# Performance work log

Measured on AMD Instinct MI355X. Metric: run time of the kernel, lower is better.

Reference implementation:

```python
import jax, jax.numpy as jnp
import numpy as np

D_MODEL = 512
D_STATE = 16
D_INNER = 2 * D_MODEL  # expand_factor=2
IN_CH = 256
B_SZ, H_SZ, W_SZ = 4, 32, 32


def setup_inputs() -> dict:
    key = jax.random.key(0)
    ks = jax.random.split(key, 24)
    f = jax.random.normal
    inp = {}
    inp["x_V"] = f(ks[0], (B_SZ, IN_CH, H_SZ, W_SZ), jnp.float32)
    inp["x_I"] = f(ks[1], (B_SZ, IN_CH, H_SZ, W_SZ), jnp.float32)
    # channel_reduce: 1x1 conv + BN (inference stats)
    inp["conv_red_w"] = f(ks[2], (D_MODEL, IN_CH), jnp.float32) * 0.05
    inp["bn_red_g"] = jnp.ones((D_MODEL,), jnp.float32)
    inp["bn_red_b"] = jnp.zeros((D_MODEL,), jnp.float32)
    inp["bn_red_m"] = jnp.zeros((D_MODEL,), jnp.float32)
    inp["bn_red_v"] = jnp.ones((D_MODEL,), jnp.float32)
    # channel_restore: 1x1 conv + BN
    inp["conv_res_w"] = f(ks[3], (IN_CH, D_MODEL), jnp.float32) * 0.05
    inp["bn_res_g"] = jnp.ones((IN_CH,), jnp.float32)
    inp["bn_res_b"] = jnp.zeros((IN_CH,), jnp.float32)
    inp["bn_res_m"] = jnp.zeros((IN_CH,), jnp.float32)
    inp["bn_res_v"] = jnp.ones((IN_CH,), jnp.float32)
    # lambda_predictor convs (1x1 on pooled features == linear)
    inp["lam_w1"] = f(ks[4], (D_MODEL // 4, D_MODEL * 2), jnp.float32) * 0.05
    inp["lam_b1"] = jnp.zeros((D_MODEL // 4,), jnp.float32)
    inp["lam_w2"] = f(ks[5], (2, D_MODEL // 4), jnp.float32) * 0.05
    inp["lam_b2"] = jnp.zeros((2,), jnp.float32)
    # two SimplifiedMamba2Blocks
    for i, p in enumerate(["V", "I"]):
        kk = jax.random.split(ks[6 + i], 6)
        inp[p + "_in_w"] = f(kk[0], (2 * D_INNER, D_MODEL), jnp.float32) * 0.03
        inp[p + "_out_w"] = f(kk[1], (D_MODEL, D_INNER), jnp.float32) * 0.03
        # A = -exp(A_log) in (-1, -0.05): stable decay
        inp[p + "_A_log"] = jnp.log(jax.random.uniform(kk[2], (D_INNER, D_STATE), jnp.float32, 0.05, 0.95))
        inp[p + "_B"] = f(kk[3], (D_INNER, D_STATE), jnp.float32) * 0.05
        inp[p + "_C"] = jnp.full((D_INNER, D_STATE), 0.01, jnp.float32)
        inp[p + "_ln_g"] = jnp.ones((D_MODEL,), jnp.float32)
        inp[p + "_ln_b"] = jnp.zeros((D_MODEL,), jnp.float32)
    inp["gate"] = jnp.asarray(0.1, jnp.float32)
    return inp


def _bn(x, g, b, m, v):
    # x: (B,C,H,W); inference-mode batchnorm
    return (x - m[:, None, None]) / jnp.sqrt(v[:, None, None] + 1e-5) * g[:, None, None] + b[:, None, None]


def _conv1x1(x, w):
    return jnp.einsum('bchw,oc->bohw', x, w)


def _ssm_scan(x_ssm, A, Bm, Cm, reverse):
    # x_ssm: (B,L,I); A,Bm,Cm: (I,S)
    bsz = x_ssm.shape[0]
    h0 = jnp.zeros((bsz, A.shape[0], A.shape[1]), x_ssm.dtype)

    def step(h, xt):  # xt: (B,I)
        h = jnp.clip(h * A + xt[:, :, None] * Bm, -10.0, 10.0)
        return h, jnp.einsum('bis,is->bi', h, Cm)

    _, ys = jax.lax.scan(step, h0, jnp.swapaxes(x_ssm, 0, 1), reverse=reverse)
    return jnp.swapaxes(ys, 0, 1)  # (B,L,I), in original time order


def _mamba(x, ln_g, ln_b, in_w, out_w, A_log, Bm, Cm):
    # LayerNorm
    mu = jnp.mean(x, -1, keepdims=True)
    var = jnp.mean((x - mu) ** 2, -1, keepdims=True)
    xn = (x - mu) / jnp.sqrt(var + 1e-5) * ln_g + ln_b
    xp = xn @ in_w.T  # (B,L,2*I)
    x_ssm, gate = jnp.split(xp, 2, axis=-1)
    A = jnp.clip(-jnp.exp(A_log), -10.0, -0.01)
    yf = _ssm_scan(x_ssm, A, Bm, Cm, False)
    yb = _ssm_scan(x_ssm, A, Bm, Cm, True)
    out = 0.5 * (yf + yb) * jax.nn.silu(gate)
    return out @ out_w.T


def reference(x_V, x_I, conv_red_w, bn_red_g, bn_red_b, bn_red_m, bn_red_v,
              conv_res_w, bn_res_g, bn_res_b, bn_res_m, bn_res_v,
              lam_w1, lam_b1, lam_w2, lam_b2,
              V_in_w, V_out_w, V_A_log, V_B, V_C, V_ln_g, V_ln_b,
              I_in_w, I_out_w, I_A_log, I_B, I_C, I_ln_g, I_ln_b, gate):
    B, _, H, W = x_V.shape
    xVr = jax.nn.relu(_bn(_conv1x1(x_V, conv_red_w), bn_red_g, bn_red_b, bn_red_m, bn_red_v))
    xIr = jax.nn.relu(_bn(_conv1x1(x_I, conv_red_w), bn_red_g, bn_red_b, bn_red_m, bn_red_v))
    # same spatial size -> adaptive pooling and [:B] slicing are identities
    conc = jnp.concatenate([xVr, xIr], axis=1)  # (B, 2*d_model, H, W)

    def lam(c):
        p = jnp.mean(c, axis=(2, 3))  # global avg pool -> (B, 2*d_model)
        h1 = jax.nn.relu(p @ lam_w1.T + lam_b1)
        return jax.nn.softmax(h1 @ lam_w2.T + lam_b2, axis=-1)  # (B,2)

    lamV = lam(conc)
    lamI = lam(conc)

    seq_V = jnp.swapaxes(xVr.reshape(B, D_MODEL, H * W), 1, 2)  # (B,L,D)
    seq_I = jnp.swapaxes(xIr.reshape(B, D_MODEL, H * W), 1, 2)

    outV_std = _mamba(seq_V, V_ln_g, V_ln_b, V_in_w, V_out_w, V_A_log, V_B, V_C)
    outI_std = _mamba(seq_I, I_ln_g, I_ln_b, I_in_w, I_out_w, I_A_log, I_B, I_C)
    outV_cross = _mamba(seq_V, V_ln_g, V_ln_b, V_in_w, V_out_w, V_A_log, jax.lax.stop_gradient(I_B), V_C)
    outI_cross = _mamba(seq_I, I_ln_g, I_ln_b, I_in_w, I_out_w, I_A_log, jax.lax.stop_gradient(V_B), I_C)

    outV = lamV[:, 0][:, None, None] * outV_std + lamV[:, 1][:, None, None] * outV_cross
    outI = lamI[:, 0][:, None, None] * outI_std + lamI[:, 1][:, None, None] * outI_cross

    featV = jnp.swapaxes(outV, 1, 2).reshape(B, D_MODEL, H, W)
    featI = jnp.swapaxes(outI, 1, 2).reshape(B, D_MODEL, H, W)
    featV = _bn(_conv1x1(featV, conv_res_w), bn_res_g, bn_res_b, bn_res_m, bn_res_v)
    featI = _bn(_conv1x1(featI, conv_res_w), bn_res_g, bn_res_b, bn_res_m, bn_res_v)

    g = jax.nn.sigmoid(gate)
    return (x_V + g * featV, x_I + g * featI)
```

## Files before the change

### kernel.cpp

```cpp
#include <hip/hip_runtime.h>
#include <hip/hip_bf16.h>
#include <math.h>

#define L_SZ 1024
#define DM   512
#define DI   1024
#define NS   16
#define CH   256

typedef float4 f4;
typedef __attribute__((ext_vector_type(8))) short short8;
typedef __attribute__((ext_vector_type(8))) unsigned short u16x8;
typedef __attribute__((ext_vector_type(4))) float f32x4;

__device__ __forceinline__ float bf2f(ushort u) {
    union { unsigned int i; float f; } x; x.i = ((unsigned int)u) << 16; return x.f;
}
__device__ __forceinline__ ushort f2bf(float f) {
    union { float f; unsigned int i; } x; x.f = f;
    unsigned int r = x.i + 0x7FFFu + ((x.i >> 16) & 1u);
    return (ushort)(r >> 16);
}
__device__ __forceinline__ uint pkbf(float a, float b) {
    union { __hip_bfloat162 h; uint u; } c;
    c.h = __float22bfloat162_rn(make_float2(a, b));
    return c.u;
}

#define GLOAD16(gp, lp) \
  __builtin_amdgcn_global_load_lds((const __attribute__((address_space(1))) void*)(gp), \
                                   (__attribute__((address_space(3))) void*)(lp), 16, 0, 0)

__global__ __launch_bounds__(256) void k_prep(
    const float* __restrict__ s0, const float* __restrict__ s1,
    const float* __restrict__ s2, const float* __restrict__ s3,
    const float* __restrict__ s4, const float* __restrict__ s5,
    ushort* __restrict__ d0, ushort* __restrict__ d1,
    ushort* __restrict__ d2, ushort* __restrict__ d3,
    ushort* __restrict__ d4, ushort* __restrict__ d5,
    const float* __restrict__ xv, const float* __restrict__ xi,
    ushort* __restrict__ xtv, ushort* __restrict__ xti,
    float* __restrict__ p, unsigned int* __restrict__ cnt)
{
    __shared__ float tile[32][36];
    const int bid = blockIdx.x;
    const int t = threadIdx.x;
    if (bid < 2304) {
        const float* s; ushort* d; int rel;
        if      (bid < 128)  { s = s0; d = d0; rel = bid; }
        else if (bid < 256)  { s = s1; d = d1; rel = bid - 128; }
        else if (bid < 1280) { s = s2; d = d2; rel = bid - 256; }
        else                 { s = s3; d = d3; rel = bid - 1280; }
        const int i = rel * 256 + t;
        f4 v = ((const f4*)s)[i];
        ushort4 o;
        o.x = f2bf(v.x); o.y = f2bf(v.y); o.z = f2bf(v.z); o.w = f2bf(v.w);
        ((ushort4*)d)[i] = o;
        return;
    }
    if (bid < 3328) {
        const int rel = (bid < 2816) ? bid - 2304 : bid - 2816;
        const float* wo = (bid < 2816) ? s4 : s5;
        ushort* wt      = (bid < 2816) ? d4 : d5;
        const int kt = rel & 31, dt = rel >> 5;
        const int d0_ = dt * 32, k0 = kt * 32;
        {
            int cc = t >> 3, ll4 = (t & 7) << 2;
            f4 v = *(const f4*)(wo + (size_t)(d0_ + cc) * 1024 + k0 + ll4);
            tile[cc][ll4 + 0] = v.x; tile[cc][ll4 + 1] = v.y;
            tile[cc][ll4 + 2] = v.z; tile[cc][ll4 + 3] = v.w;
        }
        __syncthreads();
        {
            int ll = t >> 3, cc4 = (t & 7) << 2;
            ushort4 o;
            o.x = f2bf(tile[cc4 + 0][ll]); o.y = f2bf(tile[cc4 + 1][ll]);
            o.z = f2bf(tile[cc4 + 2][ll]); o.w = f2bf(tile[cc4 + 3][ll]);
            *(ushort4*)(wt + (size_t)(k0 + ll) * 512 + d0_ + cc4) = o;
        }
        return;
    }
    if (bid < 5376) {
        const int rel = bid - 3328;
        const int l0 = (rel & 31) * 32, c0 = ((rel >> 5) & 7) * 32;
        const int z = rel >> 8;
        const int b = z & 3, st = z >> 2;
        const float* x = st ? xi : xv;
        ushort* xt = st ? xti : xtv;
        {
            int cc = t >> 3, ll4 = (t & 7) << 2;
            f4 v = *(const f4*)(x + ((size_t)(b * CH + c0 + cc)) * L_SZ + l0 + ll4);
            tile[cc][ll4 + 0] = v.x; tile[cc][ll4 + 1] = v.y;
            tile[cc][ll4 + 2] = v.z; tile[cc][ll4 + 3] = v.w;
        }
        __syncthreads();
        {
            int ll = t >> 3, cc4 = (t & 7) << 2;
            ushort4 o;
            o.x = f2bf(tile[cc4 + 0][ll]); o.y = f2bf(tile[cc4 + 1][ll]);
            o.z = f2bf(tile[cc4 + 2][ll]); o.w = f2bf(tile[cc4 + 3][ll]);
            *(ushort4*)(xt + ((size_t)(b * L_SZ + l0 + ll)) * CH + c0 + cc4) = o;
        }
        return;
    }
    const f4 z4 = {0.f, 0.f, 0.f, 0.f};
    ((f4*)p)[t]       = z4;
    ((f4*)p)[t + 256] = z4;
    ((f4*)p)[t + 512] = z4;
    ((f4*)p)[t + 768] = z4;
    if (t == 0) *cnt = 0u;
}

template<int MODE, int BM, int BN, int OS>
__global__ __launch_bounds__(256) void k_gemm(
    const ushort* __restrict__ A0, const ushort* __restrict__ A1,
    const ushort* __restrict__ B0, const ushort* __restrict__ B1,
    int K,
    float* __restrict__ o0, float* __restrict__ o1,
    ushort* __restrict__ ob0, ushort* __restrict__ ob1,
    ushort* __restrict__ sb0, ushort* __restrict__ sb1,
    const float* __restrict__ pg, const float* __restrict__ pb,
    const float* __restrict__ pm, const float* __restrict__ pv,
    const float* __restrict__ x0, const float* __restrict__ x1,
    const float* __restrict__ gate, float* __restrict__ pp)
{
    constexpr int MT   = BM / 32;
    constexpr int NT   = BN / 32;
    constexpr int ASEG = BM / 16;
    constexpr int NSEG = (BM + BN) / 16;
    constexpr int SPW  = NSEG / 4;
    __shared__ __align__(16) ushort Sl[(BM + BN) * 32];
    const int t = threadIdx.x;
    const int wv = t >> 6, lane = t & 63;
    const int n0 = blockIdx.x * BN, m0 = blockIdx.y * BM;
    const int st = blockIdx.z;
    const ushort* Ap = st ? A1 : A0;
    const ushort* Bp = st ? B1 : B0;
    const int wm = wv >> 1, wn = wv & 1;
    const int lrow = lane & 15, q = lane >> 4;
    f32x4 acc[MT][NT];
    #pragma unroll
    for (int a_ = 0; a_ < MT; ++a_)
        #pragma unroll
        for (int b_ = 0; b_ < NT; ++b_)
            acc[a_][b_] = (f32x4){0.f, 0.f, 0.f, 0.f};
    const int srow = lane >> 2;
    const int skk  = (((lane & 3) ^ ((lane >> 3) & 3)) << 3);
    const int koff = ((q ^ ((lrow >> 1) & 3)) << 3);
    for (int k0 = 0; k0 < K; k0 += 32) {
        #pragma unroll
        for (int s2 = 0; s2 < SPW; ++s2) {
            const int seg = wv * SPW + s2;
            const int grow = (seg < ASEG) ? (m0 + seg * 16 + srow)
                                          : (n0 + (seg - ASEG) * 16 + srow);
            const ushort* src = (seg < ASEG) ? Ap : Bp;
            GLOAD16(src + (size_t)grow * K + k0 + skk, &Sl[seg * 512]);
        }
        __syncthreads();
        short8 af[MT], bfr[NT];
        #pragma unroll
        for (int mt = 0; mt < MT; ++mt)
            af[mt] = *(const short8*)&Sl[(wm * (MT * 16) + mt * 16 + lrow) * 32 + koff];
        #pragma unroll
        for (int nt = 0; nt < NT; ++nt)
            bfr[nt] = *(const short8*)&Sl[(BM + wn * (NT * 16) + nt * 16 + lrow) * 32 + koff];
        #pragma unroll
        for (int mt = 0; mt < MT; ++mt)
            #pragma unroll
            for (int nt = 0; nt < NT; ++nt)
                acc[mt][nt] = __builtin_amdgcn_mfma_f32_16x16x32_bf16(af[mt], bfr[nt], acc[mt][nt], 0, 0, 0);
        __syncthreads();
    }
    if (MODE == 0) {
        ushort* sq = st ? ob1 : ob0;
        const int b = m0 >> 10;
        #pragma unroll
        for (int nt = 0; nt < NT; ++nt) {
            const int gn = n0 + wn * (NT * 16) + nt * 16 + lrow;
            const float s  = pg[gn] * rsqrtf(pv[gn] + 1e-5f);
            const float sh = pb[gn] - pm[gn] * s;
            float psum = 0.f;
            #pragma unroll
            for (int mt = 0; mt < MT; ++mt) {
                const int gm = m0 + wm * (MT * 16) + mt * 16 + q * 4;
                float v[4];
                #pragma unroll
                for (int r = 0; r < 4; ++r) {
                    v[r] = fmaxf(fmaf(acc[mt][nt][r], s, sh), 0.f);
                    psum += v[r];
                }
                const uint u01 = pkbf(v[0], v[1]);
                const uint u23 = pkbf(v[2], v[3]);
                ushort* bp = sq + (size_t)gm * DM + gn;
                bp[0]      = (ushort)u01;
                bp[DM]     = (ushort)(u01 >> 16);
                bp[2 * DM] = (ushort)u23;
                bp[3 * DM] = (ushort)(u23 >> 16);
            }
            psum += __shfl_xor(psum, 16, 64);
            psum += __shfl_xor(psum, 32, 64);
            if (q == 0)
                atomicAdd(pp + (b * 1024 + st * 512 + gn), psum * (1.0f / 1024.0f));
        }
    } else if (MODE == 1) {
        const bool isx = (n0 < 1024);
        ushort* xp = st ? ob1 : ob0;
        ushort* sp = st ? sb1 : sb0;
        #pragma unroll
        for (int nt = 0; nt < NT; ++nt) {
            const int gn = n0 + wn * (NT * 16) + nt * 16 + lrow;
            #pragma unroll
            for (int mt = 0; mt < MT; ++mt) {
                const int gm = m0 + wm * (MT * 16) + mt * 16 + q * 4;
                if (isx) {
                    const uint u01 = pkbf(acc[mt][nt][0], acc[mt][nt][1]);
                    const uint u23 = pkbf(acc[mt][nt][2], acc[mt][nt][3]);
                    ushort* bp = xp + (size_t)gm * DI + gn;
                    bp[0]      = (ushort)u01;
                    bp[DI]     = (ushort)(u01 >> 16);
                    bp[2 * DI] = (ushort)u23;
                    bp[3 * DI] = (ushort)(u23 >> 16);
                } else {
                    float sv[4];
                    #pragma unroll
                    for (int r = 0; r < 4; ++r) {
                        const float v = acc[mt][nt][r];
                        sv[r] = v / (1.f + __expf(-v));
                    }
                    const uint u01 = pkbf(sv[0], sv[1]);
                    const uint u23 = pkbf(sv[2], sv[3]);
                    ushort* bp = sp + (size_t)gm * DI + gn - 1024;
                    bp[0]      = (ushort)u01;
                    bp[DI]     = (ushort)(u01 >> 16);
                    bp[2 * DI] = (ushort)u23;
                    bp[3 * DI] = (ushort)(u23 >> 16);
                }
            }
        }
    } else if (MODE == 2) {
        ushort* fp_ = st ? ob1 : ob0;
        #pragma unroll
        for (int nt = 0; nt < NT; ++nt) {
            const int gn = n0 + wn * (NT * 16) + nt * 16 + lrow;
            #pragma unroll
            for (int mt = 0; mt < MT; ++mt) {
                const int gm = m0 + wm * (MT * 16) + mt * 16 + q * 4;
                const uint u01 = pkbf(acc[mt][nt][0], acc[mt][nt][1]);
                const uint u23 = pkbf(acc[mt][nt][2], acc[mt][nt][3]);
                ushort* bp = fp_ + (size_t)gm * OS + gn;
                bp[0]      = (ushort)u01;
                bp[OS]     = (ushort)(u01 >> 16);
                bp[2 * OS] = (ushort)u23;
                bp[3 * OS] = (ushort)(u23 >> 16);
            }
        }
    } else {
        const float* xin = st ? x1 : x0;
        float* op = st ? o1 : o0;
        const float g = 1.f / (1.f + __expf(-gate[0]));
        #pragma unroll
        for (int nt = 0; nt < NT; ++nt) {
            const int gn = n0 + wn * (NT * 16) + nt * 16 + lrow;
            const float s  = pg[gn] * rsqrtf(pv[gn] + 1e-5f);
            const float sh = pb[gn] - pm[gn] * s;
            #pragma unroll
            for (int mt = 0; mt < MT; ++mt) {
                const int gmb = m0 + wm * (MT * 16) + mt * 16 + q * 4;
                const int b = gmb >> 10, l = gmb & 1023;
                const size_t off = ((size_t)(b * CH + gn)) * L_SZ + l;
                f4 xi = *(const f4*)(xin + off);
                f4 o;
                o.x = xi.x + g * fmaf(acc[mt][nt][0], s, sh);
                o.y = xi.y + g * fmaf(acc[mt][nt][1], s, sh);
                o.z = xi.z + g * fmaf(acc[mt][nt][2], s, sh);
                o.w = xi.w + g * fmaf(acc[mt][nt][3], s, sh);
                *(f4*)(op + off) = o;
            }
        }
    }
}

__global__ __launch_bounds__(256) void k_lam(
    const float* __restrict__ p, const float* __restrict__ w1,
    const float* __restrict__ b1, const float* __restrict__ w2,
    const float* __restrict__ b2, float* __restrict__ h1,
    float* __restrict__ lam, unsigned int* __restrict__ cnt)
{
    __shared__ float lsm[8];
    __shared__ unsigned int tick;
    const int t = threadIdx.x, lane = t & 63, wv = t >> 6;
    const int idx = blockIdx.x * 4 + wv;
    const int b = idx >> 7, j = idx & 127;
    const float* pb = p + b * 1024;
    const float* wr = w1 + j * 1024;
    float s = 0.f;
    #pragma unroll
    for (int k = 0; k < 16; ++k)
        s = fmaf(pb[lane + k * 64], wr[lane + k * 64], s);
    #pragma unroll
    for (int off = 1; off < 64; off <<= 1) s += __shfl_xor(s, off, 64);
    if (lane == 0) h1[idx] = fmaxf(s + b1[j], 0.f);
    __threadfence();
    __syncthreads();
    if (t == 0) tick = atomicAdd(cnt, 1u);
    __syncthreads();
    if (tick != 127u) return;
    __threadfence();
    {
        const int g32 = t >> 5, l32 = t & 31;
        const int bb = g32 >> 1, kk = g32 & 1;
        const float* hb = h1 + bb * 128;
        const float* wr2 = w2 + kk * 128;
        float ss = 0.f;
        #pragma unroll
        for (int u = 0; u < 4; ++u)
            ss = fmaf(hb[l32 + u * 32], wr2[l32 + u * 32], ss);
        #pragma unroll
        for (int off = 1; off < 32; off <<= 1) ss += __shfl_xor(ss, off, 64);
        if (l32 == 0) lsm[g32] = ss + b2[kk];
    }
    __syncthreads();
    if (t < 4) {
        const float a0 = lsm[t * 2], a1 = lsm[t * 2 + 1];
        const float m  = fmaxf(a0, a1);
        const float e0 = __expf(a0 - m), e1 = __expf(a1 - m);
        const float inv = 1.f / (e0 + e1);
        lam[t * 2 + 0] = e0 * inv;
        lam[t * 2 + 1] = e1 * inv;
    }
}

__global__ __launch_bounds__(256) void k_ln(
    const ushort* __restrict__ seq0, const ushort* __restrict__ seq1,
    const float* __restrict__ g0, const float* __restrict__ b0,
    const float* __restrict__ g1, const float* __restrict__ b1,
    ushort* __restrict__ ln0, ushort* __restrict__ ln1)
{
    const int t = threadIdx.x, lane = t & 63, wv = t >> 6;
    const int row = blockIdx.x * 4 + wv, st = blockIdx.y;
    const ushort* seq = st ? seq1 : seq0;
    const float* gg  = st ? g1 : g0;
    const float* bb  = st ? b1 : b0;
    ushort* ln = st ? ln1 : ln0;
    const u16x8 v = *(const u16x8*)(seq + (size_t)row * DM + lane * 8);
    float f[8];
    float s = 0.f, ss = 0.f;
    #pragma unroll
    for (int i = 0; i < 8; ++i) {
        f[i] = bf2f(v[i]);
        s += f[i];
        ss = fmaf(f[i], f[i], ss);
    }
    #pragma unroll
    for (int off = 1; off < 64; off <<= 1) {
        s += __shfl_xor(s, off, 64); ss += __shfl_xor(ss, off, 64);
    }
    const float mu = s * (1.f / 512.f);
    const float rstd = rsqrtf(ss * (1.f / 512.f) - mu * mu + 1e-5f);
    const f4 gv0 = *(const f4*)(gg + lane * 8);
    const f4 gv1 = *(const f4*)(gg + lane * 8 + 4);
    const f4 bv0 = *(const f4*)(bb + lane * 8);
    const f4 bv1 = *(const f4*)(bb + lane * 8 + 4);
    const float gvv[8] = {gv0.x, gv0.y, gv0.z, gv0.w, gv1.x, gv1.y, gv1.z, gv1.w};
    const float bvv[8] = {bv0.x, bv0.y, bv0.z, bv0.w, bv1.x, bv1.y, bv1.z, bv1.w};
    u16x8 o;
    #pragma unroll
    for (int i = 0; i < 8; i += 2) {
        const uint u = pkbf(fmaf((f[i]     - mu) * rstd, gvv[i],     bvv[i]),
                            fmaf((f[i + 1] - mu) * rstd, gvv[i + 1], bvv[i + 1]));
        o[i]     = (ushort)u;
        o[i + 1] = (ushort)(u >> 16);
    }
    *(u16x8*)(ln + (size_t)row * DM + lane * 8) = o;
}

__global__ __launch_bounds__(128) void k_scan(
    const ushort* __restrict__ xsV, const ushort* __restrict__ xsI,
    const ushort* __restrict__ sgV, const ushort* __restrict__ sgI,
    const float* __restrict__ VA, const float* __restrict__ VB,
    const float* __restrict__ VC, const float* __restrict__ IA,
    const float* __restrict__ IB, const float* __restrict__ IC,
    const float* __restrict__ lam,
    ushort* __restrict__ yV, ushort* __restrict__ yI)
{
    __shared__ __align__(16) ushort xf[2][16][64];
    __shared__ __align__(16) ushort xb[2][16][64];
    __shared__ ushort yfb[32][64];
    __shared__ ushort ybb[32][64];
    const int t = threadIdx.x;
    const int shalf = t & 1;
    const int il = t >> 1;
    const int b = blockIdx.y;
    const int st = blockIdx.z >> 4, j = blockIdx.z & 15;
    const int c0 = blockIdx.x * 64;
    const ushort* xrow  = (st ? xsI : xsV) + (size_t)b * L_SZ * DI + c0;
    const ushort* sgrow = (st ? sgI : sgV) + (size_t)b * L_SZ * DI + c0;
    ushort* yrow        = (st ? yI  : yV ) + (size_t)b * L_SZ * DI + c0;
    const float* Alog = st ? IA : VA;
    const float* Cm   = st ? IC : VC;
    const float* Bown = st ? IB : VB;
    const float* Both = st ? VB : IB;
    const float lam0 = lam[b * 2 + 0], lam1 = lam[b * 2 + 1];
    float a[8], w[8], gf[8], gb[8];
    const int base = (c0 + il) * NS + shalf * 8;
    #pragma unroll
    for (int s = 0; s < 8; ++s) {
        a[s] = fminf(fmaxf(-__expf(Alog[base + s]), -10.f), -0.01f);
        w[s] = 0.5f * Cm[base + s] * fmaf(lam0, Bown[base + s], lam1 * Both[base + s]);
        gf[s] = 0.f; gb[s] = 0.f;
    }
    const int row0 = j << 6;
    const int srow = t >> 3;
    const int scol = (t & 7) << 3;
    {
        int rf = row0 - 64 + srow;          rf = max(0, min(1023, rf));
        GLOAD16(xrow + (size_t)rf * DI + scol, &xf[0][srow][0]);
        int rb = row0 + 127 - srow;         rb = max(0, min(1023, rb));
        GLOAD16(xrow + (size_t)rb * DI + scol, &xb[0][srow][0]);
    }
    __syncthreads();
    for (int si = 0; si < 8; ++si) {
        const int buf = si & 1;
        if (si < 7) {
            const int base2 = (si + 1) * 16;
            int rf = row0 - 64 + base2 + srow;  rf = max(0, min(1023, rf));
            GLOAD16(xrow + (size_t)rf * DI + scol, &xf[buf ^ 1][srow][0]);
            int rb = row0 + 127 - base2 - srow; rb = max(0, min(1023, rb));
            GLOAD16(xrow + (size_t)rb * DI + scol, &xb[buf ^ 1][srow][0]);
        }
        if (si == 4) {
            if (j == 0) {
                for (int s = 0; s < 8; ++s) gf[s] = 0.f;
            }
            if (j == 15) {
                for (int s = 0; s < 8; ++s) gb[s] = 0.f;
            }
        }
        if (si < 4) {
            #pragma unroll
            for (int n = 0; n < 16; ++n) {
                const float vf = bf2f(xf[buf][n][il]);
                const float vb = bf2f(xb[buf][n][il]);
                #pragma unroll
                for (int s = 0; s < 8; ++s) {
                    gf[s] = fmaf(a[s], gf[s], vf);
                    gb[s] = fmaf(a[s], gb[s], vb);
                }
            }
        } else if (si < 6) {
            const int mb = (si - 4) * 16;
            #pragma unroll
            for (int n = 0; n < 16; ++n) {
                const float vf = bf2f(xf[buf][n][il]);
                const float vb = bf2f(xb[buf][n][il]);
                float yf = 0.f, yb = 0.f;
                #pragma unroll
                for (int s = 0; s < 8; ++s) {
                    gf[s] = fmaf(a[s], gf[s], vf);
                    yf    = fmaf(gf[s], w[s], yf);
                    gb[s] = fmaf(a[s], gb[s], vb);
                    yb    = fmaf(gb[s], w[s], yb);
                }
                yf += __shfl_xor(yf, 1, 64);
                yb += __shfl_xor(yb, 1, 64);
                const int m = mb + n;
                ushort* qq = shalf ? &ybb[31 - m][0] : &yfb[m][0];
                qq[il] = f2bf(shalf ? yb : yf);
            }
        } else {
            const int mb = (si - 6) * 16 + 32;
            #pragma unroll
            for (int n = 0; n < 16; ++n) {
                const float vf = bf2f(xf[buf][n][il]);
                const float vb = bf2f(xb[buf][n][il]);
                float yf = 0.f, yb = 0.f;
                #pragma unroll
                for (int s = 0; s < 8; ++s) {
                    gf[s] = fmaf(a[s], gf[s], vf);
                    yf    = fmaf(gf[s], w[s], yf);
                    gb[s] = fmaf(a[s], gb[s], vb);
                    yb    = fmaf(gb[s], w[s], yb);
                }
                yf += __shfl_xor(yf, 1, 64);
                yb += __shfl_xor(yb, 1, 64);
                const int m = mb + n;
                const int rF = row0 + m;
                const int rB = row0 + 63 - m;
                const int r  = shalf ? rB : rF;
                const ushort* pq = shalf ? &yfb[63 - m][0] : &ybb[m - 32][0];
                const float own  = shalf ? yb : yf;
                const float z = (own + bf2f(pq[il]))
                              * bf2f(sgrow[(size_t)r * DI + il]);
                yrow[(size_t)r * DI + il] = f2bf(z);
            }
        }
        __syncthreads();
    }
}

extern "C" void kernel_launch(void* const* d_in, const int* in_sizes, int n_in,
                              void* d_out, int out_size, void* d_ws, size_t ws_size,
                              hipStream_t stream)
{
    const float* xV       = (const float*)d_in[0];
    const float* xI       = (const float*)d_in[1];
    const float* convredw = (const float*)d_in[2];
    const float* bnredg   = (const float*)d_in[3];
    const float* bnredb   = (const float*)d_in[4];
    const float* bnredm   = (const float*)d_in[5];
    const float* bnredv   = (const float*)d_in[6];
    const float* convresw = (const float*)d_in[7];
    const float* bnresg   = (const float*)d_in[8];
    const float* bnresb   = (const float*)d_in[9];
    const float* bnresm   = (const float*)d_in[10];
    const float* bnresv   = (const float*)d_in[11];
    const float* lamw1    = (const float*)d_in[12];
    const float* lamb1    = (const float*)d_in[13];
    const float* lamw2    = (const float*)d_in[14];
    const float* lamb2    = (const float*)d_in[15];
    const float* Vinw     = (const float*)d_in[16];
    const float* Voutw    = (const float*)d_in[17];
    const float* VAlog    = (const float*)d_in[18];
    const float* VB       = (const float*)d_in[19];
    const float* VC       = (const float*)d_in[20];
    const float* Vlng     = (const float*)d_in[21];
    const float* Vlnb     = (const float*)d_in[22];
    const float* Iinw     = (const float*)d_in[23];
    const float* Ioutw    = (const float*)d_in[24];
    const float* IAlog    = (const float*)d_in[25];
    const float* IB       = (const float*)d_in[26];
    const float* IC       = (const float*)d_in[27];
    const float* Ilng     = (const float*)d_in[28];
    const float* Ilnb     = (const float*)d_in[29];
    const float* gate     = (const float*)d_in[30];

    char* W = (char*)d_ws;
    const size_t MB = 1048576;
    ushort* seqV  = (ushort*)(W + 0);
    ushort* seqI  = (ushort*)(W + 4  * MB);
    float*  p     = (float*)(W + 8 * MB);
    float*  lam   = (float*)(W + 8 * MB + 16384);
    float*  h1    = (float*)(W + 8 * MB + 32768);
    unsigned int* cnt = (unsigned int*)(W + 8 * MB + 49152);
    ushort* sgV   = (ushort*)(W + 17 * MB);
    ushort* sgI   = (ushort*)(W + 25 * MB);
    ushort* yV    = (ushort*)(W + 33 * MB);
    ushort* yI    = (ushort*)(W + 41 * MB);
    ushort* wred  = (ushort*)(W + 65 * MB);
    ushort* wres  = (ushort*)(W + 65 * MB + 262144);
    ushort* winV  = (ushort*)(W + 66 * MB);
    ushort* winI  = (ushort*)(W + 68 * MB);
    ushort* woTv  = (ushort*)(W + 70 * MB);
    ushort* woTi  = (ushort*)(W + 71 * MB);
    ushort* xtV   = (ushort*)(W + 72 * MB);
    ushort* xtI   = (ushort*)(W + 74 * MB);
    ushort* lnV   = (ushort*)(W + 76 * MB);
    ushort* lnI   = (ushort*)(W + 80 * MB);
    ushort* xsV   = (ushort*)(W + 84 * MB);
    ushort* xsI   = (ushort*)(W + 92 * MB);
    ushort* wcombV = (ushort*)(W + 100 * MB);
    ushort* wcombI = (ushort*)(W + 100 * MB + 524288);
    float*  outp  = (float*)d_out;

    k_prep<<<dim3(5377), 256, 0, stream>>>(
        convredw, convresw, Vinw, Iinw, Voutw, Ioutw,
        wred, wres, winV, winI, woTv, woTi,
        xV, xI, xtV, xtI, p, cnt);
    k_gemm<2, 64, 64, 1024><<<dim3(16, 4, 2), 256, 0, stream>>>(
        wres, wres, woTv, woTi, 512,
        nullptr, nullptr, wcombV, wcombI, nullptr, nullptr,
        nullptr, nullptr, nullptr, nullptr, nullptr, nullptr, nullptr, nullptr);
    k_gemm<0, 128, 64, 512><<<dim3(8, 32, 2), 256, 0, stream>>>(xtV, xtI, wred, wred, 256,
        nullptr, nullptr, seqV, seqI, nullptr, nullptr,
        bnredg, bnredb, bnredm, bnredv, nullptr, nullptr, nullptr, p);
    k_lam<<<128, 256, 0, stream>>>(p, lamw1, lamb1, lamw2, lamb2, h1, lam, cnt);
    k_ln<<<dim3(1024, 2), 256, 0, stream>>>(seqV, seqI, Vlng, Vlnb, Ilng, Ilnb, lnV, lnI);
    k_gemm<1, 128, 128, 512><<<dim3(16, 32, 2), 256, 0, stream>>>(lnV, lnI, winV, winI, 512,
        nullptr, nullptr, xsV, xsI, sgV, sgI,
        nullptr, nullptr, nullptr, nullptr, nullptr, nullptr, nullptr, nullptr);
    k_scan<<<dim3(16, 4, 32), 128, 0, stream>>>(xsV, xsI, sgV, sgI,
        VAlog, VB, VC, IAlog, IB, IC, lam, yV, yI);
    k_gemm<3, 64, 64, 512><<<dim3(4, 64, 2), 256, 0, stream>>>(yV, yI, wcombV, wcombI, 1024,
        outp, outp + 1048576, nullptr, nullptr, nullptr, nullptr,
        bnresg, bnresb, bnresm, bnresv, xV, xI, gate, nullptr);
}
```

Before: 246.9 us.

## Double-buffer GEMM LDS loads, transpose MODE1 stores, prefetch scan gate into LDS

The GEMM main loop now uses two LDS buffers and prefetches the next K tile while running MFMAs on the current one. Explicit vmcnt waits and raw barriers replace __syncthreads. For MODE 1, the MFMA operands are swapped so each lane holds contiguous output columns, which allows packed 8-byte stores instead of four strided 2-byte stores. The scan kernel prefetches the SiLU gate rows into swizzled LDS during earlier stages instead of reading them from global memory in the output loop. These changes rely on hand-counted vmcnt values, which must match the number of outstanding loads exactly.

```diff
diff --git a/kernel.cpp b/kernel.cpp
--- a/kernel.cpp
+++ b/kernel.cpp
@@ -129,7 +129,7 @@
     constexpr int ASEG = BM / 16;
     constexpr int NSEG = (BM + BN) / 16;
     constexpr int SPW  = NSEG / 4;
-    __shared__ __align__(16) ushort Sl[(BM + BN) * 32];
+    __shared__ __align__(16) ushort Sl[2][(BM + BN) * 32];
     const int t = threadIdx.x;
     const int wv = t >> 6, lane = t & 63;
     const int n0 = blockIdx.x * BN, m0 = blockIdx.y * BM;
@@ -147,29 +147,52 @@
     const int srow = lane >> 2;
     const int skk  = (((lane & 3) ^ ((lane >> 3) & 3)) << 3);
     const int koff = ((q ^ ((lrow >> 1) & 3)) << 3);
+    #pragma unroll
+    for (int s2 = 0; s2 < SPW; ++s2) {
+        const int seg = wv * SPW + s2;
+        const int grow = (seg < ASEG) ? (m0 + seg * 16 + srow)
+                                      : (n0 + (seg - ASEG) * 16 + srow);
+        const ushort* src = (seg < ASEG) ? Ap : Bp;
+        GLOAD16(src + (size_t)grow * K + skk, &Sl[0][seg * 512]);
+    }
+    int cur = 0;
     for (int k0 = 0; k0 < K; k0 += 32) {
-        #pragma unroll
-        for (int s2 = 0; s2 < SPW; ++s2) {
-            const int seg = wv * SPW + s2;
-            const int grow = (seg < ASEG) ? (m0 + seg * 16 + srow)
-                                          : (n0 + (seg - ASEG) * 16 + srow);
-            const ushort* src = (seg < ASEG) ? Ap : Bp;
-            GLOAD16(src + (size_t)grow * K + k0 + skk, &Sl[seg * 512]);
-        }
-        __syncthreads();
+        if (k0 + 32 < K) {
+            #pragma unroll
+            for (int s2 = 0; s2 < SPW; ++s2) {
+                const int seg = wv * SPW + s2;
+                const int grow = (seg < ASEG) ? (m0 + seg * 16 + srow)
+                                              : (n0 + (seg - ASEG) * 16 + srow);
+                const ushort* src = (seg < ASEG) ? Ap : Bp;
+                GLOAD16(src + (size_t)grow * K + (k0 + 32) + skk, &Sl[cur ^ 1][seg * 512]);
+            }
+            if constexpr (SPW == 2)      asm volatile("s_waitcnt vmcnt(2)" ::: "memory");
+            else if constexpr (SPW == 3) asm volatile("s_waitcnt vmcnt(3)" ::: "memory");
+            else                         asm volatile("s_waitcnt vmcnt(4)" ::: "memory");
+        } else {
+            asm volatile("s_waitcnt vmcnt(0)" ::: "memory");
+        }
+        __builtin_amdgcn_s_barrier();
         short8 af[MT], bfr[NT];
         #pragma unroll
         for (int mt = 0; mt < MT; ++mt)
-            af[mt] = *(const short8*)&Sl[(wm * (MT * 16) + mt * 16 + lrow) * 32 + koff];
+            af[mt] = *(const short8*)&Sl[cur][(wm * (MT * 16) + mt * 16 + lrow) * 32 + koff];
         #pragma unroll
         for (int nt = 0; nt < NT; ++nt)
-            bfr[nt] = *(const short8*)&Sl[(BM + wn * (NT * 16) + nt * 16 + lrow) * 32 + koff];
+            bfr[nt] = *(const short8*)&Sl[cur][(BM + wn * (NT * 16) + nt * 16 + lrow) * 32 + koff];
         #pragma unroll
         for (int mt = 0; mt < MT; ++mt)
             #pragma unroll
-            for (int nt = 0; nt < NT; ++nt)
-                acc[mt][nt] = __builtin_amdgcn_mfma_f32_16x16x32_bf16(af[mt], bfr[nt], acc[mt][nt], 0, 0, 0);
-        __syncthreads();
+            for (int nt = 0; nt < NT; ++nt) {
+                if constexpr (MODE == 1)
+                    acc[mt][nt] = __builtin_amdgcn_mfma_f32_16x16x32_bf16(bfr[nt], af[mt], acc[mt][nt], 0, 0, 0);
+                else
+                    acc[mt][nt] = __builtin_amdgcn_mfma_f32_16x16x32_bf16(af[mt], bfr[nt], acc[mt][nt], 0, 0, 0);
+            }
+        asm volatile("s_waitcnt lgkmcnt(0)" ::: "memory");
+        __builtin_amdgcn_sched_barrier(0);
+        __builtin_amdgcn_s_barrier();
+        cur ^= 1;
     }
     if (MODE == 0) {
         ushort* sq = st ? ob1 : ob0;
@@ -207,19 +230,15 @@
         ushort* xp = st ? ob1 : ob0;
         ushort* sp = st ? sb1 : sb0;
         #pragma unroll
-        for (int nt = 0; nt < NT; ++nt) {
-            const int gn = n0 + wn * (NT * 16) + nt * 16 + lrow;
-            #pragma unroll
-            for (int mt = 0; mt < MT; ++mt) {
-                const int gm = m0 + wm * (MT * 16) + mt * 16 + q * 4;
+        for (int mt = 0; mt < MT; ++mt) {
+            const int gm = m0 + wm * (MT * 16) + mt * 16 + lrow;
+            #pragma unroll
+            for (int nt = 0; nt < NT; ++nt) {
+                const int gnb = n0 + wn * (NT * 16) + nt * 16 + q * 4;
                 if (isx) {
                     const uint u01 = pkbf(acc[mt][nt][0], acc[mt][nt][1]);
                     const uint u23 = pkbf(acc[mt][nt][2], acc[mt][nt][3]);
-                    ushort* bp = xp + (size_t)gm * DI + gn;
-                    bp[0]      = (ushort)u01;
-                    bp[DI]     = (ushort)(u01 >> 16);
-                    bp[2 * DI] = (ushort)u23;
-                    bp[3 * DI] = (ushort)(u23 >> 16);
+                    *(uint2*)(xp + (size_t)gm * DI + gnb) = make_uint2(u01, u23);
                 } else {
                     float sv[4];
                     #pragma unroll
@@ -229,11 +248,7 @@
                     }
                     const uint u01 = pkbf(sv[0], sv[1]);
                     const uint u23 = pkbf(sv[2], sv[3]);
-                    ushort* bp = sp + (size_t)gm * DI + gn - 1024;
-                    bp[0]      = (ushort)u01;
-                    bp[DI]     = (ushort)(u01 >> 16);
-                    bp[2 * DI] = (ushort)u23;
-                    bp[3 * DI] = (ushort)(u23 >> 16);
+                    *(uint2*)(sp + (size_t)gm * DI + gnb - 1024) = make_uint2(u01, u23);
                 }
             }
         }
@@ -385,8 +400,10 @@
 {
     __shared__ __align__(16) ushort xf[2][16][64];
     __shared__ __align__(16) ushort xb[2][16][64];
-    __shared__ ushort yfb[32][64];
-    __shared__ ushort ybb[32][64];
+    __shared__ __align__(16) ushort sgl[64][64];
+    __shared__ ushort ybuf[4096 + 32];
+#define YFB(m) (ybuf + (m) * 64)
+#define YBB(m) (ybuf + 2080 + (m) * 64)
     const int t = threadIdx.x;
     const int shalf = t & 1;
     const int il = t >> 1;
@@ -412,13 +429,13 @@
     const int row0 = j << 6;
     const int srow = t >> 3;
     const int scol = (t & 7) << 3;
+    const int scolS = scol ^ ((srow & 1) << 5);
     {
         int rf = row0 - 64 + srow;          rf = max(0, min(1023, rf));
         GLOAD16(xrow + (size_t)rf * DI + scol, &xf[0][srow][0]);
         int rb = row0 + 127 - srow;         rb = max(0, min(1023, rb));
         GLOAD16(xrow + (size_t)rb * DI + scol, &xb[0][srow][0]);
     }
-    __syncthreads();
     for (int si = 0; si < 8; ++si) {
         const int buf = si & 1;
         if (si < 7) {
@@ -428,6 +445,18 @@
             int rb = row0 + 127 - base2 - srow; rb = max(0, min(1023, rb));
             GLOAD16(xrow + (size_t)rb * DI + scol, &xb[buf ^ 1][srow][0]);
         }
+        if (si == 4) {
+            GLOAD16(sgrow + (size_t)(row0 + srow) * DI + scolS,      &sgl[srow][0]);
+            GLOAD16(sgrow + (size_t)(row0 + 16 + srow) * DI + scolS, &sgl[16 + srow][0]);
+        } else if (si == 5) {
+            GLOAD16(sgrow + (size_t)(row0 + 32 + srow) * DI + scolS, &sgl[32 + srow][0]);
+            GLOAD16(sgrow + (size_t)(row0 + 48 + srow) * DI + scolS, &sgl[48 + srow][0]);
+        }
+        if (si == 4)      asm volatile("s_waitcnt vmcnt(4)"  ::: "memory");
+        else if (si == 5) asm volatile("s_waitcnt vmcnt(6)"  ::: "memory");
+        else if (si < 7)  asm volatile("s_waitcnt vmcnt(2)"  ::: "memory");
+        else              asm volatile("s_waitcnt vmcnt(16)" ::: "memory");
+        __builtin_amdgcn_s_barrier();
         if (si == 4) {
             if (j == 0) {
                 for (int s = 0; s < 8; ++s) gf[s] = 0.f;
@@ -464,7 +493,7 @@
                 yf += __shfl_xor(yf, 1, 64);
                 yb += __shfl_xor(yb, 1, 64);
                 const int m = mb + n;
-                ushort* qq = shalf ? &ybb[31 - m][0] : &yfb[m][0];
+                ushort* qq = shalf ? (YBB(31 - m)) : (YFB(m));
                 qq[il] = f2bf(shalf ? yb : yf);
             }
         } else {
@@ -487,15 +516,20 @@
                 const int rF = row0 + m;
                 const int rB = row0 + 63 - m;
                 const int r  = shalf ? rB : rF;
-                const ushort* pq = shalf ? &yfb[63 - m][0] : &ybb[m - 32][0];
+                const int rr = r - row0;
+                const ushort* pq = shalf ? YFB(63 - m) : YBB(m - 32);
                 const float own  = shalf ? yb : yf;
                 const float z = (own + bf2f(pq[il]))
-                              * bf2f(sgrow[(size_t)r * DI + il]);
+                              * bf2f(sgl[rr][il ^ ((rr & 1) << 5)]);
                 yrow[(size_t)r * DI + il] = f2bf(z);
             }
         }
-        __syncthreads();
-    }
+        asm volatile("s_waitcnt lgkmcnt(0)" ::: "memory");
+        __builtin_amdgcn_sched_barrier(0);
+        __builtin_amdgcn_s_barrier();
+    }
+#undef YFB
+#undef YBB
 }
 
 extern "C" void kernel_launch(void* const* d_in, const int* in_sizes, int n_in,
```

Result: faster. 241.7 us (-2.1%).
